# Kernel tuning notes

Measured on AMD Instinct MI355X. Metric: run time of the kernel, lower is better.

The kernel has to match this reference:

```python
import jax, jax.numpy as jnp
import numpy as np

N_NODES, N_EDGES = 50000, 800000
D_NODE, D_EDGE, N_CLASSES, N_HEADS = 64, 64, 40, 4


def setup_inputs() -> dict:
    key = jax.random.key(0)
    ks = jax.random.split(key, 20)
    g = lambda k, shp: (jax.random.normal(k, shp, jnp.float32) * (1.0 / np.sqrt(shp[0])))
    inp = {
        "nodes": jax.random.normal(ks[0], (N_NODES, D_NODE), jnp.float32),
        "edges": jax.random.normal(ks[1], (N_EDGES, D_EDGE), jnp.float32),
        "edge_index": jax.random.randint(ks[2], (2, N_EDGES), 0, N_NODES, jnp.int32),
        # NodeAttention params
        "Wq_n": g(ks[3], (D_NODE, D_NODE)),
        "Wk_n": g(ks[4], (D_NODE, D_NODE)),
        "We_n": g(ks[5], (D_EDGE, D_NODE)),
        "Wv_n": g(ks[6], (D_NODE, D_NODE)),
        "Wo_n": g(ks[7], (D_NODE, D_NODE)),
        # EdgeAttention params
        "Wq_e": g(ks[8], (D_EDGE, D_EDGE)),
        "Wk_e": g(ks[9], (D_EDGE, D_EDGE)),
        "Wn_e": g(ks[10], (D_NODE, D_EDGE)),
        "Wv_e": g(ks[11], (D_EDGE, D_EDGE)),
        "Wo_e": g(ks[12], (D_EDGE, D_EDGE)),
        # classifier: Linear(2*d_node+d_edge -> d_edge), GELU, Linear(d_edge -> num_classes)
        "W1": g(ks[13], (2 * D_NODE + D_EDGE, D_EDGE)),
        "b1": jnp.zeros((D_EDGE,), jnp.float32),
        "W2": g(ks[14], (D_EDGE, N_CLASSES)),
        "b2": jnp.zeros((N_CLASSES,), jnp.float32),
    }
    return inp


def _segment_softmax(scores, seg, num_segments):
    # scores: [E, H], seg: [E] -> softmax over edges within each segment
    m = jax.ops.segment_max(scores, seg, num_segments)
    ex = jnp.exp(scores - m[seg])
    den = jax.ops.segment_sum(ex, seg, num_segments)
    return ex / (den[seg] + 1e-9)


def _forward(nodes, edges, edge_index, Wq_n, Wk_n, We_n, Wv_n, Wo_n,
             Wq_e, Wk_e, Wn_e, Wv_e, Wo_e, W1, b1, W2, b2):
    src, tgt = edge_index[0], edge_index[1]
    E = edges.shape[0]
    N = nodes.shape[0]
    Dh_n = D_NODE // N_HEADS
    Dh_e = D_EDGE // N_HEADS

    # ---- NodeAttention: nodes attend over incoming edges ----
    q = (nodes @ Wq_n).reshape(N, N_HEADS, Dh_n)
    k = ((nodes @ Wk_n)[src] + edges @ We_n).reshape(E, N_HEADS, Dh_n)
    v = (nodes @ Wv_n)[src].reshape(E, N_HEADS, Dh_n)
    s_n = (q[tgt] * k).sum(-1) / jnp.sqrt(jnp.float32(Dh_n))  # [E, H]
    a_n = _segment_softmax(s_n, tgt, N)
    msg = jax.ops.segment_sum(a_n[..., None] * v, tgt, N).reshape(N, D_NODE)
    new_nodes = nodes + msg @ Wo_n

    # ---- EdgeAttention: edges attend among edges sharing a source node ----
    qe = (edges @ Wq_e).reshape(E, N_HEADS, Dh_e)
    ke = (edges @ Wk_e + nodes[src] @ Wn_e).reshape(E, N_HEADS, Dh_e)
    ve = (edges @ Wv_e).reshape(E, N_HEADS, Dh_e)
    s_e = (qe * ke).sum(-1) / jnp.sqrt(jnp.float32(Dh_e))  # [E, H]
    a_e = _segment_softmax(s_e, src, N)
    pooled = jax.ops.segment_sum(a_e[..., None] * ve, src, N).reshape(N, D_EDGE)
    new_edges = edges + pooled[src] @ Wo_e

    # ---- edge-indexed gather + concat + 2-layer GELU MLP classifier ----
    combined = jnp.concatenate([new_nodes[src], new_nodes[tgt], new_edges], axis=-1)
    h = jax.nn.gelu(combined @ W1 + b1)
    return h @ W2 + b2  # [E, num_classes]


def reference(nodes, edges, edge_index, Wq_n, Wk_n, We_n, Wv_n, Wo_n,
              Wq_e, Wk_e, Wn_e, Wv_e, Wo_e, W1, b1, W2, b2):
    return _forward(nodes, edges, edge_index, Wq_n, Wk_n, We_n, Wv_n, Wo_n,
                    Wq_e, Wk_e, Wn_e, Wv_e, Wo_e, W1, b1, W2, b2)
```

## Files before the change

### kernel.cpp

```cpp
#include <hip/hip_runtime.h>
#include <cstdint>
#include <cstddef>

typedef unsigned short u16t;
typedef __attribute__((ext_vector_type(8))) short bf16x8;
typedef __attribute__((ext_vector_type(4))) float f32x4;

#define NNODES 50000
#define NEDGES 800000
#define NP 50176

#define MFMA(a, b, c) __builtin_amdgcn_mfma_f32_16x16x32_bf16((a), (b), (c), 0, 0, 0)

__device__ inline float b2f(short s) {
    union { float f; unsigned int u; } c;
    c.u = ((unsigned int)(unsigned short)s) << 16;
    return c.f;
}
__device__ inline short f2b(float f) {
    union { float f; unsigned int u; } c; c.f = f;
    unsigned int u = c.u;
    unsigned int r = (u + 0x7FFFu + ((u >> 16) & 1u)) >> 16;
    return (short)(unsigned short)r;
}
__device__ inline f32x4 zero4() { f32x4 z = {0.f, 0.f, 0.f, 0.f}; return z; }

__device__ inline bf16x8 ld8f(const float* p) {
    float4 a = *(const float4*)p;
    float4 b = *(const float4*)(p + 4);
    bf16x8 r;
    r[0] = f2b(a.x); r[1] = f2b(a.y); r[2] = f2b(a.z); r[3] = f2b(a.w);
    r[4] = f2b(b.x); r[5] = f2b(b.y); r[6] = f2b(b.z); r[7] = f2b(b.w);
    return r;
}

__device__ inline float gelu_f(float x) {
    float u = 0.7978845608028654f * (x + 0.044715f * x * x * x);
    float e = __expf(2.f * u);
    return 0.5f * x * (2.f - 2.f / (e + 1.f));
}

__device__ inline float tree16(float* a, int l) {
#pragma unroll
    for (int b = 0; b < 4; ++b) {
        const int m = 1 << b;
        const bool up = (l & m) != 0;
#pragma unroll
        for (int j = 0; j < (8 >> b); ++j) {
            float keep = up ? a[2 * j + 1] : a[2 * j];
            float send = up ? a[2 * j] : a[2 * j + 1];
            a[j] = keep + __shfl_xor(send, m);
        }
    }
    return a[0];
}

__device__ inline int wscan_incl(int v) {
    int l = threadIdx.x & 63;
#pragma unroll
    for (int d = 1; d < 64; d <<= 1) {
        int t = __shfl_up(v, d);
        if (l >= d) v += t;
    }
    return v;
}

__global__ void k_zero(int* __restrict__ cnt) {
    int i = blockIdx.x * 256 + threadIdx.x;
    cnt[i] = 0;
}

__global__ void k_hist(const int* __restrict__ eidx, int* __restrict__ cnt) {
    int e = blockIdx.x * 256 + threadIdx.x;
    int sr = eidx[e], tg = eidx[NEDGES + e];
    atomicAdd(&cnt[tg], 1);
    atomicAdd(&cnt[NP + sr], 1);
}

__global__ void k_scan_blk(const int* __restrict__ cnt, int* __restrict__ incl,
                           int* __restrict__ tot) {
    __shared__ int wsum[4];
    int i = blockIdx.x * 256 + threadIdx.x;
    int v = cnt[i];
    int sc = wscan_incl(v);
    int w = threadIdx.x >> 6;
    if ((threadIdx.x & 63) == 63) wsum[w] = sc;
    __syncthreads();
    int off = 0;
    for (int k = 0; k < w; ++k) off += wsum[k];
    incl[i] = sc + off;
    if (threadIdx.x == 255) tot[blockIdx.x] = sc + off;
}

__global__ void k_scan_top(const int* __restrict__ tot, int* __restrict__ ttop) {
    __shared__ int wsum[8];
    int i = threadIdx.x;
    int v = (i < 392) ? tot[i] : 0;
    int sc = wscan_incl(v);
    int w = threadIdx.x >> 6;
    if ((threadIdx.x & 63) == 63) wsum[w] = sc;
    __syncthreads();
    int off = 0;
    for (int k = 0; k < w; ++k) off += wsum[k];
    if (i < 392) ttop[i] = sc + off - v;
}

__global__ void k_scan_add(const int* __restrict__ cnt, const int* __restrict__ incl,
                           const int* __restrict__ ttop, int* __restrict__ ofs,
                           int* __restrict__ cur) {
    int i = blockIdx.x * 256 + threadIdx.x;
    int v = incl[i] - cnt[i] + ttop[blockIdx.x];
    ofs[i] = v; cur[i] = v;
}

__global__ void k_fill(const int* __restrict__ eidx, int* __restrict__ cur,
                       int* __restrict__ perm) {
    int e = blockIdx.x * 256 + threadIdx.x;
    int sr = eidx[e], tg = eidx[NEDGES + e];
    perm[atomicAdd(&cur[tg], 1)] = e;
    perm[atomicAdd(&cur[NP + sr], 1)] = e;
}

__global__ __launch_bounds__(256) void k_node_proj(
        const float* __restrict__ nodes,
        const float* __restrict__ Wq, const float* __restrict__ Wk,
        const float* __restrict__ Wv, const float* __restrict__ Wn,
        u16t* __restrict__ qn, u16t* __restrict__ kn,
        u16t* __restrict__ vn, u16t* __restrict__ nWn) {
    __shared__ __align__(16) u16t wt[256 * 72];
    {
        const float* Ws[4] = {Wq, Wk, Wv, Wn};
        for (int g = 0; g < 4; ++g) {
            const float* W = Ws[g];
            u16t* dst = wt + g * 64 * 72;
            for (int idx = threadIdx.x; idx < 4096; idx += 256) {
                int n = idx & 63, k = idx >> 6;
                dst[n * 72 + k] = (u16t)f2b(W[idx]);
            }
        }
    }
    __syncthreads();
    int l = threadIdx.x & 63, w = threadIdx.x >> 6;
    int q = l >> 4, c = l & 15;
    int r0 = blockIdx.x * 256 + w * 64;

    bf16x8 A[4][2];
#pragma unroll
    for (int st = 0; st < 4; ++st) {
        int row = r0 + st * 16 + c;
        if (row >= NNODES) row = NNODES - 1;
#pragma unroll
        for (int ks = 0; ks < 2; ++ks)
            A[st][ks] = ld8f(nodes + (size_t)row * 64 + ks * 32 + q * 8);
    }
    u16t* outs[4] = {qn, kn, vn, nWn};
    for (int cg = 0; cg < 4; ++cg) {
        bf16x8 B[2][4];
#pragma unroll
        for (int ks = 0; ks < 2; ++ks)
#pragma unroll
            for (int t = 0; t < 4; ++t)
                B[ks][t] = *(const bf16x8*)(wt + (cg * 64 + t * 16 + c) * 72 + ks * 32 + q * 8);
        float scale = (cg == 0) ? 0.25f : 1.0f;
        u16t* out = outs[cg];
#pragma unroll
        for (int st = 0; st < 4; ++st) {
            f32x4 acc[4];
#pragma unroll
            for (int t = 0; t < 4; ++t) acc[t] = zero4();
#pragma unroll
            for (int ks = 0; ks < 2; ++ks)
#pragma unroll
                for (int t = 0; t < 4; ++t)
                    acc[t] = MFMA(A[st][ks], B[ks][t], acc[t]);
#pragma unroll
            for (int r = 0; r < 4; ++r) {
                int row = r0 + st * 16 + q * 4 + r;
                if (row < NNODES) {
#pragma unroll
                    for (int t = 0; t < 4; ++t)
                        out[(size_t)row * 64 + t * 16 + c] = (u16t)f2b(acc[t][r] * scale);
                }
            }
        }
    }
}

__global__ __launch_bounds__(256) void k_edge_scores(
        const float* __restrict__ edges, const int* __restrict__ eidx,
        const float* __restrict__ WeN, const float* __restrict__ WqE, const float* __restrict__ WkE,
        const u16t* __restrict__ qn, const u16t* __restrict__ kn, const u16t* __restrict__ nWn,
        float* __restrict__ s_n, float* __restrict__ s_e) {
    __shared__ __align__(16) u16t wt[192 * 72];
    for (int idx = threadIdx.x; idx < 4096; idx += 256) {
        int n = idx & 63, k = idx >> 6;
        wt[n * 72 + k]         = (u16t)f2b(WeN[idx]);
        wt[(64 + n) * 72 + k]  = (u16t)f2b(0.25f * WqE[idx]);
        wt[(128 + n) * 72 + k] = (u16t)f2b(WkE[idx]);
    }
    __syncthreads();
    int l = threadIdx.x & 63, w = threadIdx.x >> 6;
    int q = l >> 4, c = l & 15;
    int e0 = blockIdx.x * 256 + w * 64;

    for (int st = 0; st < 4; ++st) {
        int ebase = e0 + st * 16;
        int eA = ebase + c;
        bf16x8 A0 = ld8f(edges + (size_t)eA * 64 + q * 8);
        bf16x8 A1 = ld8f(edges + (size_t)eA * 64 + 32 + q * 8);

        int sr_[4], tg_[4];
#pragma unroll
        for (int r = 0; r < 4; ++r) {
            int e = ebase + q * 4 + r;
            sr_[r] = eidx[e];
            tg_[r] = eidx[NEDGES + e];
        }

        f32x4 aQe[4], aKe[4];
#pragma unroll
        for (int t = 0; t < 4; ++t) { aQe[t] = zero4(); aKe[t] = zero4(); }
#pragma unroll
        for (int t = 0; t < 4; ++t) {
            const u16t* b1 = wt + (64 + t * 16 + c) * 72;
            const u16t* b2 = wt + (128 + t * 16 + c) * 72;
            aQe[t] = MFMA(A0, *(const bf16x8*)(b1 + q * 8), aQe[t]);
            aQe[t] = MFMA(A1, *(const bf16x8*)(b1 + 32 + q * 8), aQe[t]);
            aKe[t] = MFMA(A0, *(const bf16x8*)(b2 + q * 8), aKe[t]);
            aKe[t] = MFMA(A1, *(const bf16x8*)(b2 + 32 + q * 8), aKe[t]);
        }
        float pe[16];
#pragma unroll
        for (int r = 0; r < 4; ++r)
#pragma unroll
            for (int t = 0; t < 4; ++t) {
                int col = t * 16 + c;
                float ng = b2f((short)nWn[(size_t)sr_[r] * 64 + col]);
                pe[r * 4 + t] = aQe[t][r] * (aKe[t][r] + ng);
            }
        s_e[(size_t)ebase * 4 + l] = __expf(tree16(pe, l));

        f32x4 aWe[4];
#pragma unroll
        for (int t = 0; t < 4; ++t) aWe[t] = zero4();
#pragma unroll
        for (int t = 0; t < 4; ++t) {
            const u16t* b0 = wt + (t * 16 + c) * 72;
            aWe[t] = MFMA(A0, *(const bf16x8*)(b0 + q * 8), aWe[t]);
            aWe[t] = MFMA(A1, *(const bf16x8*)(b0 + 32 + q * 8), aWe[t]);
        }
        float pn[16];
#pragma unroll
        for (int r = 0; r < 4; ++r)
#pragma unroll
            for (int t = 0; t < 4; ++t) {
                int col = t * 16 + c;
                float qg = b2f((short)qn[(size_t)tg_[r] * 64 + col]);
                float kg = b2f((short)kn[(size_t)sr_[r] * 64 + col]);
                pn[r * 4 + t] = qg * (kg + aWe[t][r]);
            }
        s_n[(size_t)ebase * 4 + l] = __expf(tree16(pn, l));
    }
}

__global__ __launch_bounds__(256) void k_gather(
        const float* __restrict__ edges, const int* __restrict__ eidx,
        const float* __restrict__ WvE,
        const int* __restrict__ ofs, const int* __restrict__ cnt,
        const int* __restrict__ perm,
        const float* __restrict__ s_n, const float* __restrict__ s_e,
        const u16t* __restrict__ vn,
        float* __restrict__ msg, float* __restrict__ pooled) {
    __shared__ __align__(16) u16t wt[64 * 72];
    for (int idx = threadIdx.x; idx < 4096; idx += 256) {
        int n = idx & 63, k = idx >> 6;
        wt[n * 72 + k] = (u16t)f2b(WvE[idx]);
    }
    __syncthreads();
    int l = threadIdx.x & 63;
    int q = l >> 4, c = l & 15;
    int gw = (blockIdx.x * 256 + (int)threadIdx.x) >> 6;
    if (gw >= NNODES) return;

    {
        int o0 = ofs[gw], n0 = cnt[gw];
        float acc = 0.f, den = 0.f;
        int e = (n0 > 0) ? perm[o0] : 0;
        for (int j = 0; j < n0; ++j) {
            int sr = eidx[e];
            int en = (j + 1 < n0) ? perm[o0 + j + 1] : 0;
            float a = s_n[(size_t)e * 4 + q];
            den += a;
            acc += a * b2f((short)vn[(size_t)sr * 64 + l]);
            e = en;
        }
        msg[(size_t)gw * 64 + l] = acc / (den + 1e-9f);
    }

    {
        int o1 = ofs[NP + gw], n1 = cnt[NP + gw];
        float part[4] = {0.f, 0.f, 0.f, 0.f};
        float dpart[4] = {0.f, 0.f, 0.f, 0.f};
        for (int j0 = 0; j0 < n1; j0 += 16) {
            int rem = n1 - j0;
            int cc = (c < rem) ? c : (rem - 1);
            int eC = perm[o1 + j0 + cc];
            bf16x8 A0 = ld8f(edges + (size_t)eC * 64 + q * 8);
            bf16x8 A1 = ld8f(edges + (size_t)eC * 64 + 32 + q * 8);
            f32x4 acc4[4];
#pragma unroll
            for (int t = 0; t < 4; ++t) acc4[t] = zero4();
#pragma unroll
            for (int t = 0; t < 4; ++t) {
                const u16t* bp = wt + (t * 16 + c) * 72;
                acc4[t] = MFMA(A0, *(const bf16x8*)(bp + q * 8), acc4[t]);
                acc4[t] = MFMA(A1, *(const bf16x8*)(bp + 32 + q * 8), acc4[t]);
            }
#pragma unroll
            for (int r = 0; r < 4; ++r) {
                int row = q * 4 + r;
                int eR = __shfl(eC, row);
                float4 a4;
                if (row < rem) a4 = *(const float4*)(s_e + (size_t)eR * 4);
                else           { a4.x = 0.f; a4.y = 0.f; a4.z = 0.f; a4.w = 0.f; }
                float ar[4] = {a4.x, a4.y, a4.z, a4.w};
#pragma unroll
                for (int t = 0; t < 4; ++t) {
                    part[t] += ar[t] * acc4[t][r];
                    dpart[t] += ar[t];
                }
            }
        }
#pragma unroll
        for (int t = 0; t < 4; ++t) {
            part[t] += __shfl_xor(part[t], 16);
            part[t] += __shfl_xor(part[t], 32);
            dpart[t] += __shfl_xor(dpart[t], 16);
            dpart[t] += __shfl_xor(dpart[t], 32);
        }
        float pv = (q == 0) ? part[0] : (q == 1) ? part[1] : (q == 2) ? part[2] : part[3];
        float dv = (q == 0) ? dpart[0] : (q == 1) ? dpart[1] : (q == 2) ? dpart[2] : dpart[3];
        pooled[(size_t)gw * 64 + l] = pv / (dv + 1e-9f);
    }
}

__global__ __launch_bounds__(256) void k_node_update(
        const float* __restrict__ Ain, const float* __restrict__ W,
        const float* __restrict__ base, u16t* __restrict__ out) {
    __shared__ __align__(16) u16t wt[64 * 72];
    for (int idx = threadIdx.x; idx < 4096; idx += 256) {
        int n = idx & 63, k = idx >> 6;
        wt[n * 72 + k] = (u16t)f2b(W[idx]);
    }
    __syncthreads();
    int l = threadIdx.x & 63, w = threadIdx.x >> 6;
    int q = l >> 4, c = l & 15;
    int r0 = blockIdx.x * 256 + w * 64;
    bf16x8 B[2][4];
#pragma unroll
    for (int ks = 0; ks < 2; ++ks)
#pragma unroll
        for (int t = 0; t < 4; ++t)
            B[ks][t] = *(const bf16x8*)(wt + (t * 16 + c) * 72 + ks * 32 + q * 8);
    for (int st = 0; st < 4; ++st) {
        int row = r0 + st * 16 + c;
        if (row >= NNODES) row = NNODES - 1;
        bf16x8 A[2];
#pragma unroll
        for (int ks = 0; ks < 2; ++ks)
            A[ks] = ld8f(Ain + (size_t)row * 64 + ks * 32 + q * 8);
        f32x4 acc[4];
#pragma unroll
        for (int t = 0; t < 4; ++t) acc[t] = zero4();
#pragma unroll
        for (int t = 0; t < 4; ++t) {
            acc[t] = MFMA(A[0], B[0][t], acc[t]);
            acc[t] = MFMA(A[1], B[1][t], acc[t]);
        }
#pragma unroll
        for (int r = 0; r < 4; ++r) {
            int rw = r0 + st * 16 + q * 4 + r;
            if (rw < NNODES) {
#pragma unroll
                for (int t = 0; t < 4; ++t) {
                    int col = t * 16 + c;
                    float v = acc[t][r];
                    if (base) v += base[(size_t)rw * 64 + col];
                    out[(size_t)rw * 64 + col] = (u16t)f2b(v);
                }
            }
        }
    }
}

__global__ __launch_bounds__(256) void k_classifier(
        const float* __restrict__ edges, const int* __restrict__ eidx,
        const u16t* __restrict__ newN, const u16t* __restrict__ pWo,
        const float* __restrict__ W1, const float* __restrict__ b1,
        const float* __restrict__ W2, const float* __restrict__ b2,
        float* __restrict__ out) {
    __shared__ __align__(16) u16t wt1[64 * 200];
    __shared__ __align__(16) u16t wt2[48 * 72];
    __shared__ __align__(16) u16t hbuf[4][16 * 72];
    for (int idx = threadIdx.x; idx < 192 * 64; idx += 256) {
        int n = idx & 63, k = idx >> 6;
        wt1[n * 200 + k] = (u16t)f2b(W1[idx]);
    }
    for (int idx = threadIdx.x; idx < 48 * 64; idx += 256) {
        int n = idx % 48, k = idx / 48;
        wt2[n * 72 + k] = (n < 40) ? (u16t)f2b(W2[k * 40 + n]) : (u16t)0;
    }
    __syncthreads();
    int l = threadIdx.x & 63, w = threadIdx.x >> 6;
    int q = l >> 4, c = l & 15;
    int e0 = blockIdx.x * 256 + w * 64;

    bf16x8 B1[6][4];
#pragma unroll
    for (int ks = 0; ks < 6; ++ks)
#pragma unroll
        for (int t = 0; t < 4; ++t)
            B1[ks][t] = *(const bf16x8*)(wt1 + (t * 16 + c) * 200 + ks * 32 + q * 8);
    bf16x8 B2[2][3];
#pragma unroll
    for (int ks = 0; ks < 2; ++ks)
#pragma unroll
        for (int t = 0; t < 3; ++t)
            B2[ks][t] = *(const bf16x8*)(wt2 + (t * 16 + c) * 72 + ks * 32 + q * 8);

    for (int st = 0; st < 4; ++st) {
        int em = e0 + st * 16 + c;
        int srm = eidx[em], tgm = eidx[NEDGES + em];
        bf16x8 A[6];
#pragma unroll
        for (int ks = 0; ks < 2; ++ks) {
            A[ks]     = *(const bf16x8*)(newN + (size_t)srm * 64 + ks * 32 + q * 8);
            A[2 + ks] = *(const bf16x8*)(newN + (size_t)tgm * 64 + ks * 32 + q * 8);
            const float* ep = edges + (size_t)em * 64 + ks * 32 + q * 8;
            float4 x0 = *(const float4*)ep;
            float4 x1 = *(const float4*)(ep + 4);
            bf16x8 y = *(const bf16x8*)(pWo + (size_t)srm * 64 + ks * 32 + q * 8);
            bf16x8 z;
            z[0] = f2b(x0.x + b2f(y[0])); z[1] = f2b(x0.y + b2f(y[1]));
            z[2] = f2b(x0.z + b2f(y[2])); z[3] = f2b(x0.w + b2f(y[3]));
            z[4] = f2b(x1.x + b2f(y[4])); z[5] = f2b(x1.y + b2f(y[5]));
            z[6] = f2b(x1.z + b2f(y[6])); z[7] = f2b(x1.w + b2f(y[7]));
            A[4 + ks] = z;
        }
        f32x4 acc1[4];
#pragma unroll
        for (int t = 0; t < 4; ++t) acc1[t] = zero4();
#pragma unroll
        for (int ks = 0; ks < 6; ++ks)
#pragma unroll
            for (int t = 0; t < 4; ++t)
                acc1[t] = MFMA(A[ks], B1[ks][t], acc1[t]);
#pragma unroll
        for (int t = 0; t < 4; ++t) {
            float bb = b1[t * 16 + c];
#pragma unroll
            for (int r = 0; r < 4; ++r) {
                float x = acc1[t][r] + bb;
                hbuf[w][(q * 4 + r) * 72 + t * 16 + c] = (u16t)f2b(gelu_f(x));
            }
        }
        bf16x8 A2[2];
#pragma unroll
        for (int ks = 0; ks < 2; ++ks)
            A2[ks] = *(const bf16x8*)(&hbuf[w][c * 72 + ks * 32 + q * 8]);
        f32x4 acc2[3];
#pragma unroll
        for (int t = 0; t < 3; ++t) acc2[t] = zero4();
#pragma unroll
        for (int ks = 0; ks < 2; ++ks)
#pragma unroll
            for (int t = 0; t < 3; ++t)
                acc2[t] = MFMA(A2[ks], B2[ks][t], acc2[t]);
#pragma unroll
        for (int r = 0; r < 4; ++r) {
            int e = e0 + st * 16 + q * 4 + r;
#pragma unroll
            for (int t = 0; t < 3; ++t) {
                int col = t * 16 + c;
                if (col < 40)
                    out[(size_t)e * 40 + col] = acc2[t][r] + b2[col];
            }
        }
    }
}

extern "C" void kernel_launch(void* const* d_in, const int* in_sizes, int n_in,
                              void* d_out, int out_size, void* d_ws, size_t ws_size,
                              hipStream_t stream) {
    if (n_in < 17) return;
    const float* nodes = (const float*)d_in[0];
    const float* edges = (const float*)d_in[1];
    const int*   eidx  = (const int*)d_in[2];
    const float* Wq_n = (const float*)d_in[3];
    const float* Wk_n = (const float*)d_in[4];
    const float* We_n = (const float*)d_in[5];
    const float* Wv_n = (const float*)d_in[6];
    const float* Wo_n = (const float*)d_in[7];
    const float* Wq_e = (const float*)d_in[8];
    const float* Wk_e = (const float*)d_in[9];
    const float* Wn_e = (const float*)d_in[10];
    const float* Wv_e = (const float*)d_in[11];
    const float* Wo_e = (const float*)d_in[12];
    const float* W1   = (const float*)d_in[13];
    const float* b1   = (const float*)d_in[14];
    const float* W2   = (const float*)d_in[15];
    const float* b2   = (const float*)d_in[16];
    float* out = (float*)d_out;

    float* ws = (float*)d_ws;
    size_t o = 0;
    u16t* qn  = (u16t*)(ws + o); o += (size_t)NP * 32;
    u16t* kn  = (u16t*)(ws + o); o += (size_t)NP * 32;
    u16t* vn  = (u16t*)(ws + o); o += (size_t)NP * 32;
    u16t* nWn = (u16t*)(ws + o); o += (size_t)NP * 32;
    float* s_n = ws + o; o += (size_t)NEDGES * 4;
    float* s_e = ws + o; o += (size_t)NEDGES * 4;
    float* msg    = ws + o; o += (size_t)NP * 64;
    float* pooled = ws + o; o += (size_t)NP * 64;
    u16t* newN = (u16t*)(ws + o); o += (size_t)NP * 32;
    u16t* pWo  = (u16t*)(ws + o); o += (size_t)NP * 32;
    int* cnt  = (int*)(ws + o); o += (size_t)2 * NP;
    int* incl = (int*)(ws + o); o += (size_t)2 * NP;
    int* ofs  = (int*)(ws + o); o += (size_t)2 * NP;
    int* cur  = (int*)(ws + o); o += (size_t)2 * NP;
    int* tot  = (int*)(ws + o); o += 512;
    int* ttop = (int*)(ws + o); o += 512;
    int* perm = (int*)(ws + o); o += (size_t)2 * NEDGES;
    if (ws_size < o * sizeof(float)) return;

    k_zero<<<392, 256, 0, stream>>>(cnt);
    k_hist<<<3125, 256, 0, stream>>>(eidx, cnt);
    k_scan_blk<<<392, 256, 0, stream>>>(cnt, incl, tot);
    k_scan_top<<<1, 512, 0, stream>>>(tot, ttop);
    k_scan_add<<<392, 256, 0, stream>>>(cnt, incl, ttop, ofs, cur);
    k_fill<<<3125, 256, 0, stream>>>(eidx, cur, perm);
    k_node_proj<<<196, 256, 0, stream>>>(nodes, Wq_n, Wk_n, Wv_n, Wn_e, qn, kn, vn, nWn);
    k_edge_scores<<<3125, 256, 0, stream>>>(edges, eidx, We_n, Wq_e, Wk_e,
                                            qn, kn, nWn, s_n, s_e);
    k_gather<<<12500, 256, 0, stream>>>(edges, eidx, Wv_e, ofs, cnt, perm,
                                        s_n, s_e, vn, msg, pooled);
    k_node_update<<<196, 256, 0, stream>>>(msg, Wo_n, nodes, newN);
    k_node_update<<<196, 256, 0, stream>>>(pooled, Wo_e, nullptr, pWo);
    k_classifier<<<3125, 256, 0, stream>>>(edges, eidx, newN, pWo, W1, b1, W2, b2, out);
}
```

Baseline: 1.055 ms.

## Split gather kernel, pool raw edges per head and fold Wv_e·Wo_e

Splits the combined gather into two kernels. The node-attention kernel now stages 64 edge indices and scores in shared memory per batch instead of walking a serial dependent perm chain. The edge-attention kernel no longer runs an MFMA projection per edge. It pools raw edge features weighted by each head's attention into a 256-wide per-node buffer. A precomputed per-head Wv_e·Wo_e matrix (256x64) is then applied in a new node-level GEMM. This moves the V projection from edges to nodes and aliases the new buffer onto workspace that is dead by then. In exchange it adds a 4x larger intermediate and an extra kernel launch.

```diff
diff --git a/kernel.cpp b/kernel.cpp
--- a/kernel.cpp
+++ b/kernel.cpp
@@ -79,29 +79,29 @@
 
 __global__ void k_scan_blk(const int* __restrict__ cnt, int* __restrict__ incl,
                            int* __restrict__ tot) {
-    __shared__ int wsum[4];
+    __shared__ int wsumS[4];
     int i = blockIdx.x * 256 + threadIdx.x;
     int v = cnt[i];
     int sc = wscan_incl(v);
     int w = threadIdx.x >> 6;
-    if ((threadIdx.x & 63) == 63) wsum[w] = sc;
+    if ((threadIdx.x & 63) == 63) wsumS[w] = sc;
     __syncthreads();
     int off = 0;
-    for (int k = 0; k < w; ++k) off += wsum[k];
+    for (int k = 0; k < w; ++k) off += wsumS[k];
     incl[i] = sc + off;
     if (threadIdx.x == 255) tot[blockIdx.x] = sc + off;
 }
 
 __global__ void k_scan_top(const int* __restrict__ tot, int* __restrict__ ttop) {
-    __shared__ int wsum[8];
+    __shared__ int wsumS[8];
     int i = threadIdx.x;
     int v = (i < 392) ? tot[i] : 0;
     int sc = wscan_incl(v);
     int w = threadIdx.x >> 6;
-    if ((threadIdx.x & 63) == 63) wsum[w] = sc;
+    if ((threadIdx.x & 63) == 63) wsumS[w] = sc;
     __syncthreads();
     int off = 0;
-    for (int k = 0; k < w; ++k) off += wsum[k];
+    for (int k = 0; k < w; ++k) off += wsumS[k];
     if (i < 392) ttop[i] = sc + off - v;
 }
 
@@ -119,6 +119,18 @@
     int sr = eidx[e], tg = eidx[NEDGES + e];
     perm[atomicAdd(&cur[tg], 1)] = e;
     perm[atomicAdd(&cur[NP + sr], 1)] = e;
+}
+
+__global__ void k_wbig(const float* __restrict__ Wv, const float* __restrict__ Wo,
+                       float* __restrict__ Wbig) {
+    int i = blockIdx.x * 256 + threadIdx.x;
+    int row = i >> 6, d = i & 63;
+    int h = row >> 6, k = row & 63;
+    float s = 0.f;
+#pragma unroll
+    for (int j = 0; j < 16; ++j)
+        s += Wv[k * 64 + h * 16 + j] * Wo[(h * 16 + j) * 64 + d];
+    Wbig[i] = s;
 }
 
 __global__ __launch_bounds__(256) void k_node_proj(
@@ -263,85 +275,83 @@
     }
 }
 
-__global__ __launch_bounds__(256) void k_gather(
-        const float* __restrict__ edges, const int* __restrict__ eidx,
-        const float* __restrict__ WvE,
+__global__ __launch_bounds__(256) void k_gatherA(
+        const int* __restrict__ eidx,
         const int* __restrict__ ofs, const int* __restrict__ cnt,
-        const int* __restrict__ perm,
-        const float* __restrict__ s_n, const float* __restrict__ s_e,
-        const u16t* __restrict__ vn,
-        float* __restrict__ msg, float* __restrict__ pooled) {
-    __shared__ __align__(16) u16t wt[64 * 72];
-    for (int idx = threadIdx.x; idx < 4096; idx += 256) {
-        int n = idx & 63, k = idx >> 6;
-        wt[n * 72 + k] = (u16t)f2b(WvE[idx]);
-    }
-    __syncthreads();
-    int l = threadIdx.x & 63;
-    int q = l >> 4, c = l & 15;
+        const int* __restrict__ perm, const float* __restrict__ s_n,
+        const u16t* __restrict__ vn, float* __restrict__ msg) {
+    __shared__ float sw[4][64 * 4];
+    __shared__ int   sx[4][64];
+    int l = threadIdx.x & 63, w = threadIdx.x >> 6;
+    int q = l >> 4;
     int gw = (blockIdx.x * 256 + (int)threadIdx.x) >> 6;
     if (gw >= NNODES) return;
 
-    {
-        int o0 = ofs[gw], n0 = cnt[gw];
-        float acc = 0.f, den = 0.f;
-        int e = (n0 > 0) ? perm[o0] : 0;
-        for (int j = 0; j < n0; ++j) {
-            int sr = eidx[e];
-            int en = (j + 1 < n0) ? perm[o0 + j + 1] : 0;
-            float a = s_n[(size_t)e * 4 + q];
+    int o0 = ofs[gw], n0 = cnt[gw];
+    float acc = 0.f, den = 0.f;
+    for (int j0 = 0; j0 < n0; j0 += 64) {
+        int m = n0 - j0; if (m > 64) m = 64;
+        if (l < m) {
+            int e = perm[o0 + j0 + l];
+            sx[w][l] = eidx[e];
+            *(float4*)&sw[w][l * 4] = *(const float4*)(s_n + (size_t)e * 4);
+        }
+        int jj = 0;
+        for (; jj + 3 < m; jj += 4) {
+#pragma unroll
+            for (int u = 0; u < 4; ++u) {
+                float a = sw[w][(jj + u) * 4 + q];
+                int sr = sx[w][jj + u];
+                den += a;
+                acc += a * b2f((short)vn[(size_t)sr * 64 + l]);
+            }
+        }
+        for (; jj < m; ++jj) {
+            float a = sw[w][jj * 4 + q];
+            int sr = sx[w][jj];
             den += a;
             acc += a * b2f((short)vn[(size_t)sr * 64 + l]);
-            e = en;
-        }
-        msg[(size_t)gw * 64 + l] = acc / (den + 1e-9f);
-    }
-
-    {
-        int o1 = ofs[NP + gw], n1 = cnt[NP + gw];
-        float part[4] = {0.f, 0.f, 0.f, 0.f};
-        float dpart[4] = {0.f, 0.f, 0.f, 0.f};
-        for (int j0 = 0; j0 < n1; j0 += 16) {
-            int rem = n1 - j0;
-            int cc = (c < rem) ? c : (rem - 1);
-            int eC = perm[o1 + j0 + cc];
-            bf16x8 A0 = ld8f(edges + (size_t)eC * 64 + q * 8);
-            bf16x8 A1 = ld8f(edges + (size_t)eC * 64 + 32 + q * 8);
-            f32x4 acc4[4];
-#pragma unroll
-            for (int t = 0; t < 4; ++t) acc4[t] = zero4();
-#pragma unroll
-            for (int t = 0; t < 4; ++t) {
-                const u16t* bp = wt + (t * 16 + c) * 72;
-                acc4[t] = MFMA(A0, *(const bf16x8*)(bp + q * 8), acc4[t]);
-                acc4[t] = MFMA(A1, *(const bf16x8*)(bp + 32 + q * 8), acc4[t]);
-            }
-#pragma unroll
-            for (int r = 0; r < 4; ++r) {
-                int row = q * 4 + r;
-                int eR = __shfl(eC, row);
-                float4 a4;
-                if (row < rem) a4 = *(const float4*)(s_e + (size_t)eR * 4);
-                else           { a4.x = 0.f; a4.y = 0.f; a4.z = 0.f; a4.w = 0.f; }
-                float ar[4] = {a4.x, a4.y, a4.z, a4.w};
-#pragma unroll
-                for (int t = 0; t < 4; ++t) {
-                    part[t] += ar[t] * acc4[t][r];
-                    dpart[t] += ar[t];
-                }
-            }
-        }
-#pragma unroll
-        for (int t = 0; t < 4; ++t) {
-            part[t] += __shfl_xor(part[t], 16);
-            part[t] += __shfl_xor(part[t], 32);
-            dpart[t] += __shfl_xor(dpart[t], 16);
-            dpart[t] += __shfl_xor(dpart[t], 32);
-        }
-        float pv = (q == 0) ? part[0] : (q == 1) ? part[1] : (q == 2) ? part[2] : part[3];
-        float dv = (q == 0) ? dpart[0] : (q == 1) ? dpart[1] : (q == 2) ? dpart[2] : dpart[3];
-        pooled[(size_t)gw * 64 + l] = pv / (dv + 1e-9f);
-    }
+        }
+    }
+    msg[(size_t)gw * 64 + l] = acc / (den + 1e-9f);
+}
+
+__global__ __launch_bounds__(256) void k_gatherB(
+        const float* __restrict__ edges,
+        const int* __restrict__ ofs, const int* __restrict__ cnt,
+        const int* __restrict__ perm, const float* __restrict__ s_e,
+        u16t* __restrict__ wsum4) {
+    __shared__ float sw[4][64 * 4];
+    __shared__ int   sx[4][64];
+    int l = threadIdx.x & 63, w = threadIdx.x >> 6;
+    int gw = (blockIdx.x * 256 + (int)threadIdx.x) >> 6;
+    if (gw >= NNODES) return;
+
+    int o1 = ofs[NP + gw], n1 = cnt[NP + gw];
+    float a0s = 0.f, a1s = 0.f, a2s = 0.f, a3s = 0.f;
+    float c0 = 0.f, c1 = 0.f, c2 = 0.f, c3 = 0.f;
+    for (int j0 = 0; j0 < n1; j0 += 64) {
+        int m = n1 - j0; if (m > 64) m = 64;
+        if (l < m) {
+            int e = perm[o1 + j0 + l];
+            sx[w][l] = e;
+            *(float4*)&sw[w][l * 4] = *(const float4*)(s_e + (size_t)e * 4);
+        }
+#pragma unroll 4
+        for (int jj = 0; jj < m; ++jj) {
+            int e = sx[w][jj];
+            float x = edges[(size_t)e * 64 + l];
+            float a0 = sw[w][jj * 4 + 0], a1 = sw[w][jj * 4 + 1];
+            float a2 = sw[w][jj * 4 + 2], a3 = sw[w][jj * 4 + 3];
+            a0s += a0; a1s += a1; a2s += a2; a3s += a3;
+            c0 += a0 * x; c1 += a1 * x; c2 += a2 * x; c3 += a3 * x;
+        }
+    }
+    size_t base = (size_t)gw * 256 + l;
+    wsum4[base]       = (u16t)f2b(c0 / (a0s + 1e-9f));
+    wsum4[base + 64]  = (u16t)f2b(c1 / (a1s + 1e-9f));
+    wsum4[base + 128] = (u16t)f2b(c2 / (a2s + 1e-9f));
+    wsum4[base + 192] = (u16t)f2b(c3 / (a3s + 1e-9f));
 }
 
 __global__ __launch_bounds__(256) void k_node_update(
@@ -388,6 +398,43 @@
                     if (base) v += base[(size_t)rw * 64 + col];
                     out[(size_t)rw * 64 + col] = (u16t)f2b(v);
                 }
+            }
+        }
+    }
+}
+
+__global__ __launch_bounds__(256) void k_node_update256(
+        const u16t* __restrict__ Ain, const float* __restrict__ W,
+        u16t* __restrict__ out) {
+    __shared__ __align__(16) u16t wt[64 * 264];
+    for (int idx = threadIdx.x; idx < 256 * 64; idx += 256) {
+        int n = idx & 63, k = idx >> 6;
+        wt[n * 264 + k] = (u16t)f2b(W[k * 64 + n]);
+    }
+    __syncthreads();
+    int l = threadIdx.x & 63, w = threadIdx.x >> 6;
+    int q = l >> 4, c = l & 15;
+    int r0 = blockIdx.x * 256 + w * 64;
+    for (int st = 0; st < 4; ++st) {
+        int row = r0 + st * 16 + c;
+        if (row >= NNODES) row = NNODES - 1;
+        f32x4 acc[4];
+#pragma unroll
+        for (int t = 0; t < 4; ++t) acc[t] = zero4();
+#pragma unroll
+        for (int ks = 0; ks < 8; ++ks) {
+            bf16x8 A = *(const bf16x8*)(Ain + (size_t)row * 256 + ks * 32 + q * 8);
+#pragma unroll
+            for (int t = 0; t < 4; ++t)
+                acc[t] = MFMA(A, *(const bf16x8*)(wt + (t * 16 + c) * 264 + ks * 32 + q * 8), acc[t]);
+        }
+#pragma unroll
+        for (int r = 0; r < 4; ++r) {
+            int rw = r0 + st * 16 + q * 4 + r;
+            if (rw < NNODES) {
+#pragma unroll
+                for (int t = 0; t < 4; ++t)
+                    out[(size_t)rw * 64 + t * 16 + c] = (u16t)f2b(acc[t][r]);
             }
         }
     }
@@ -514,23 +561,25 @@
 
     float* ws = (float*)d_ws;
     size_t o = 0;
-    u16t* qn  = (u16t*)(ws + o); o += (size_t)NP * 32;
-    u16t* kn  = (u16t*)(ws + o); o += (size_t)NP * 32;
-    u16t* vn  = (u16t*)(ws + o); o += (size_t)NP * 32;
-    u16t* nWn = (u16t*)(ws + o); o += (size_t)NP * 32;
-    float* s_n = ws + o; o += (size_t)NEDGES * 4;
+    u16t* vn   = (u16t*)(ws + o); o += (size_t)NP * 32;
     float* s_e = ws + o; o += (size_t)NEDGES * 4;
-    float* msg    = ws + o; o += (size_t)NP * 64;
-    float* pooled = ws + o; o += (size_t)NP * 64;
+    float* msg = ws + o; o += (size_t)NP * 64;
     u16t* newN = (u16t*)(ws + o); o += (size_t)NP * 32;
     u16t* pWo  = (u16t*)(ws + o); o += (size_t)NP * 32;
+    float* Wbig = ws + o; o += 16384;
     int* cnt  = (int*)(ws + o); o += (size_t)2 * NP;
-    int* incl = (int*)(ws + o); o += (size_t)2 * NP;
     int* ofs  = (int*)(ws + o); o += (size_t)2 * NP;
     int* cur  = (int*)(ws + o); o += (size_t)2 * NP;
+    int* incl = (int*)(ws + o); o += (size_t)2 * NP;
     int* tot  = (int*)(ws + o); o += 512;
     int* ttop = (int*)(ws + o); o += 512;
     int* perm = (int*)(ws + o); o += (size_t)2 * NEDGES;
+    size_t oG = o;
+    u16t* qn   = (u16t*)(ws + o); o += (size_t)NP * 32;
+    u16t* kn   = (u16t*)(ws + o); o += (size_t)NP * 32;
+    u16t* nWn  = (u16t*)(ws + o); o += (size_t)NP * 32;
+    float* s_n = ws + o; o += (size_t)NEDGES * 4;
+    u16t* wsum4 = (u16t*)(ws + oG);
     if (ws_size < o * sizeof(float)) return;
 
     k_zero<<<392, 256, 0, stream>>>(cnt);
@@ -539,12 +588,13 @@
     k_scan_top<<<1, 512, 0, stream>>>(tot, ttop);
     k_scan_add<<<392, 256, 0, stream>>>(cnt, incl, ttop, ofs, cur);
     k_fill<<<3125, 256, 0, stream>>>(eidx, cur, perm);
+    k_wbig<<<64, 256, 0, stream>>>(Wv_e, Wo_e, Wbig);
     k_node_proj<<<196, 256, 0, stream>>>(nodes, Wq_n, Wk_n, Wv_n, Wn_e, qn, kn, vn, nWn);
     k_edge_scores<<<3125, 256, 0, stream>>>(edges, eidx, We_n, Wq_e, Wk_e,
                                             qn, kn, nWn, s_n, s_e);
-    k_gather<<<12500, 256, 0, stream>>>(edges, eidx, Wv_e, ofs, cnt, perm,
-                                        s_n, s_e, vn, msg, pooled);
+    k_gatherA<<<12500, 256, 0, stream>>>(eidx, ofs, cnt, perm, s_n, vn, msg);
+    k_gatherB<<<12500, 256, 0, stream>>>(edges, ofs, cnt, perm, s_e, wsum4);
     k_node_update<<<196, 256, 0, stream>>>(msg, Wo_n, nodes, newN);
-    k_node_update<<<196, 256, 0, stream>>>(pooled, Wo_e, nullptr, pWo);
+    k_node_update256<<<196, 256, 0, stream>>>(wsum4, Wbig, pWo);
     k_classifier<<<3125, 256, 0, stream>>>(edges, eidx, newN, pWo, W1, b1, W2, b2, out);
 }
```

Measured after the change: 901.9 us. -14.5%, faster.
